# Kernel optimization log

Hardware: AMD Instinct MI355X
Metric: run time of the kernel (lower is better)

## Reference

```python
import jax, jax.numpy as jnp
import numpy as np

N = 131072          # events
N_OBS = 64          # observables
HID = [512, 512, 512]          # trunk hidden widths
SUB_HID = [512, 256]           # per-pair subnetwork hidden widths
P = 3                          # number of pairings


def _glorot(key, shape):
    fan_in, fan_out = shape[-2], shape[-1]
    lim = np.sqrt(6.0 / (fan_in + fan_out)).astype(np.float32)
    return jax.random.uniform(key, shape, jnp.float32, -lim, lim)


def setup_inputs() -> dict:
    key = jax.random.key(0)
    ks = jax.random.split(key, 16)
    x = jax.random.normal(ks[0], (N, N_OBS), jnp.float32)
    y = jax.random.randint(ks[1], (N,), 0, 3)
    pairs = jnp.array([[0, 1], [0, 2], [1, 2]], dtype=jnp.int32)
    # trunk params
    W0 = _glorot(ks[2], (N_OBS, HID[0])); b0 = jnp.zeros((HID[0],), jnp.float32)
    W1 = _glorot(ks[3], (HID[0], HID[1])); b1 = jnp.zeros((HID[1],), jnp.float32)
    W2 = _glorot(ks[4], (HID[1], HID[2])); b2 = jnp.zeros((HID[2],), jnp.float32)
    # stacked per-pair subnetwork params (all P subnets share shapes)
    SW0 = _glorot(ks[5], (P, HID[2], SUB_HID[0])); Sb0 = jnp.zeros((P, SUB_HID[0]), jnp.float32)
    SW1 = _glorot(ks[6], (P, SUB_HID[0], SUB_HID[1])); Sb1 = jnp.zeros((P, SUB_HID[1]), jnp.float32)
    SW2 = _glorot(ks[7], (P, SUB_HID[1], 1)); Sb2 = jnp.zeros((P, 1), jnp.float32)
    return {"x": x, "y": y, "pairs": pairs,
            "W0": W0, "b0": b0, "W1": W1, "b1": b1, "W2": W2, "b2": b2,
            "SW0": SW0, "Sb0": Sb0, "SW1": SW1, "Sb1": Sb1, "SW2": SW2, "Sb2": Sb2}


def reference(x, y, pairs, W0, b0, W1, b1, W2, b2, SW0, Sb0, SW1, Sb1, SW2, Sb2):
    relu = jax.nn.relu
    # Trunk. Note: in the torch module with dropout_prob>0, the first Linear sits at
    # layer index 1, so the activation is applied to the raw input as well (eval-mode
    # dropout == identity). We reproduce that exactly.
    h = relu(x) @ W0 + b0
    h = relu(h) @ W1 + b1
    repr_ = relu(h) @ W2 + b2                      # [N, HID[-1]]

    # Per-pair membership masks (jit-safe stand-in for the variable-size gather):
    # mask[p, n] = True iff y[n] is one of the two labels of pairing p.
    mask = (y[None, :] == pairs[:, 0:1]) | (y[None, :] == pairs[:, 1:2])  # [P, N] bool

    # Per-pair RatioModel subnetworks, batched over the pair dim.
    # Same activation-before-every-Linear pattern as the trunk (dropout indices).
    hs = jnp.einsum('nd,pdh->pnh', relu(repr_), SW0) + Sb0[:, None, :]
    hs = jnp.einsum('pnh,phk->pnk', relu(hs), SW1) + Sb1[:, None, :]
    logit = jnp.einsum('pnk,pko->pno', relu(hs), SW2) + Sb2[:, None, :]  # [P, N, 1]
    s_hat = jnp.clip(jax.nn.sigmoid(logit[..., 0]), 1e-9, None)          # [P, N]
    r_hat = (1.0 - s_hat) / s_hat                                        # [P, N]

    maskf = mask.astype(s_hat.dtype)
    return repr_, r_hat * maskf, s_hat * maskf, mask
```

## Files before the change

kernel.cpp:

```cpp
#include <hip/hip_runtime.h>
#include <stdint.h>

#define NE 131072

typedef __attribute__((ext_vector_type(8))) short bf16x8;
typedef __attribute__((ext_vector_type(4))) float f32x4;

static __device__ __forceinline__ unsigned short f2bf(float f) {
  unsigned u = __float_as_uint(f);
  u += 0x7FFF + ((u >> 16) & 1);
  return (unsigned short)(u >> 16);
}
static __device__ __forceinline__ float bf2f(unsigned short h) {
  return __uint_as_float((unsigned)h << 16);
}
static __device__ __forceinline__ void gload_lds16(const void* g, void* l) {
  __builtin_amdgcn_global_load_lds(
      (const __attribute__((address_space(1))) unsigned*)g,
      (__attribute__((address_space(3))) unsigned*)l, 16, 0, 0);
}

__global__ void weight_prep(const float* __restrict__ W0, const float* __restrict__ W1,
                            const float* __restrict__ W2, const float* __restrict__ SW0,
                            const float* __restrict__ SW1, const float* __restrict__ SW2,
                            unsigned short* W0t, unsigned short* W1t,
                            unsigned short* W2t, unsigned short* SW0t,
                            unsigned short* SW1t, unsigned short* SW2b) {
  __shared__ float tile[32][33];
  const int u = blockIdx.y;
  const float* src; unsigned short* dst; int K, Nc;
  if (u == 0)      { src = W0;  dst = W0t;  K = 64;  Nc = 512; }
  else if (u == 1) { src = W1;  dst = W1t;  K = 512; Nc = 512; }
  else if (u == 2) { src = W2;  dst = W2t;  K = 512; Nc = 512; }
  else if (u < 6)  { int p = u - 3; src = SW0 + (long)p * 512 * 512; dst = SW0t + (long)p * 512 * 512; K = 512; Nc = 512; }
  else if (u < 9)  { int p = u - 6; src = SW1 + (long)p * 512 * 256; dst = SW1t + (long)p * 256 * 512; K = 512; Nc = 256; }
  else             { int p = u - 9; src = SW2 + (long)p * 256;       dst = SW2b + (long)p * 256;       K = 256; Nc = 1; }
  const int tkn = K >> 5;
  const int tk = blockIdx.x % tkn, tn = blockIdx.x / tkn;
  if (tn >= ((Nc + 31) >> 5)) return;
  const int k0 = tk * 32, n0 = tn * 32;
  const int tx = threadIdx.x & 31, ty = threadIdx.x >> 5;
  if (n0 + tx < Nc)
#pragma unroll
    for (int j = 0; j < 4; ++j)
      tile[ty * 4 + j][tx] = src[(long)(k0 + ty * 4 + j) * Nc + n0 + tx];
  __syncthreads();
#pragma unroll
  for (int j = 0; j < 4; ++j) {
    int n = n0 + ty * 4 + j;
    if (n < Nc) dst[(long)n * K + k0 + tx] = f2bf(tile[tx][ty * 4 + j]);
  }
}

__global__ void relu_cvt_x(const float4* __restrict__ x,
                           ushort4* __restrict__ xb) {
  int i = blockIdx.x * blockDim.x + threadIdx.x;
  float4 v = x[i];
  ushort4 o;
  o.x = f2bf(fmaxf(v.x, 0.f));
  o.y = f2bf(fmaxf(v.y, 0.f));
  o.z = f2bf(fmaxf(v.z, 0.f));
  o.w = f2bf(fmaxf(v.w, 0.f));
  xb[i] = o;
}

__global__ __launch_bounds__(512, 4) void gemmP(
    const unsigned short* __restrict__ A, long aZ,
    const unsigned short* __restrict__ Bt, long bZ,
    const float* __restrict__ bias, long biasZ,
    float* __restrict__ outF,
    unsigned short* __restrict__ outA, long cZ,
    int K, int Nc,
    const unsigned short* __restrict__ w2, long w2Z,
    float* __restrict__ PB, long pbZ, int r0) {
  __shared__ unsigned short lds[3 * 12288];
  __shared__ float part[4][256];
  const int z = blockIdx.z;
  A += (long)z * aZ;
  Bt += (long)z * bZ;
  bias += (long)z * biasZ;
  if (outA) outA += (long)z * cZ;
  if (w2) { w2 += (long)z * w2Z; PB += (long)z * pbZ; }

  const int tid = threadIdx.x, wave = tid >> 6, lane = tid & 63;
  const int wm = wave >> 2, wn = wave & 3;
  const int lr = lane & 15, lh = lane >> 4;
  const long brow = (long)blockIdx.x * 256;
  const int bcol = blockIdx.y * 128;
  const int nk = K >> 5;
  const int axr = (lh ^ ((lr >> 1) & 3)) * 8;

  f32x4 acc[8][2];
#pragma unroll
  for (int m = 0; m < 8; ++m)
#pragma unroll
    for (int n = 0; n < 2; ++n) acc[m][n] = (f32x4){0.f, 0.f, 0.f, 0.f};

  auto STAGE = [&](int t) {
    if (t >= nk) return;
    unsigned short* dst = &lds[(t % 3) * 12288];
    const int k0 = t << 5;
#pragma unroll
    for (int i = 0; i < 2; ++i) {
      const int cb = i * 512 + wave * 64;
      const int c = cb + lane;
      const int r = c >> 2;
      const int kc = (c & 3) ^ ((r >> 1) & 3);
      gload_lds16(A + (brow + r) * (long)K + k0 + kc * 8, &dst[cb * 8]);
    }
    {
      const int cb = wave * 64;
      const int c = cb + lane;
      const int r = c >> 2;
      const int kc = (c & 3) ^ ((r >> 1) & 3);
      gload_lds16(Bt + (long)(bcol + r) * K + k0 + kc * 8,
                  &dst[(1024 + cb) * 8]);
    }
  };

  STAGE(0);
  STAGE(1);

  for (int t = 0; t < nk; ++t) {
    if (t < nk - 1)
      asm volatile("s_waitcnt vmcnt(3)" ::: "memory");
    else
      asm volatile("s_waitcnt vmcnt(0)" ::: "memory");
    __builtin_amdgcn_s_barrier();
    __builtin_amdgcn_sched_barrier(0);
    const unsigned short* buf = &lds[(t % 3) * 12288];
    bf16x8 a[8], b[2];
#pragma unroll
    for (int m = 0; m < 8; ++m)
      a[m] = *(const bf16x8*)&buf[(wm * 128 + m * 16 + lr) * 32 + axr];
#pragma unroll
    for (int n = 0; n < 2; ++n)
      b[n] = *(const bf16x8*)&buf[1024 * 8 + (wn * 32 + n * 16 + lr) * 32 + axr];
    STAGE(t + 2);
    __builtin_amdgcn_s_setprio(1);
#pragma unroll
    for (int m = 0; m < 8; ++m)
#pragma unroll
      for (int n = 0; n < 2; ++n)
        acc[m][n] =
            __builtin_amdgcn_mfma_f32_16x16x32_bf16(a[m], b[n], acc[m][n], 0, 0, 0);
    __builtin_amdgcn_s_setprio(0);
  }

  float bv[2];
#pragma unroll
  for (int n = 0; n < 2; ++n) bv[n] = bias[bcol + wn * 32 + n * 16 + lr];

  if (!w2) {
#pragma unroll
    for (int m = 0; m < 8; ++m) {
#pragma unroll
      for (int r = 0; r < 4; ++r) {
        long e = brow + wm * 128 + m * 16 + lh * 4 + r;
#pragma unroll
        for (int n = 0; n < 2; ++n) {
          int oc = bcol + wn * 32 + n * 16 + lr;
          float v = acc[m][n][r] + bv[n];
          if (outF) outF[e * Nc + oc] = v;
          if (outA) outA[e * Nc + oc] = f2bf(fmaxf(v, 0.f));
        }
      }
    }
  } else {
    float w2v[2];
#pragma unroll
    for (int n = 0; n < 2; ++n) w2v[n] = bf2f(w2[bcol + wn * 32 + n * 16 + lr]);
#pragma unroll
    for (int m = 0; m < 8; ++m) {
#pragma unroll
      for (int r = 0; r < 4; ++r) {
        float s = 0.f;
#pragma unroll
        for (int n = 0; n < 2; ++n)
          s += fmaxf(acc[m][n][r] + bv[n], 0.f) * w2v[n];
#pragma unroll
        for (int off = 1; off < 16; off <<= 1) s += __shfl_xor(s, off);
        if (lr == 0) part[wn][wm * 128 + m * 16 + lh * 4 + r] = s;
      }
    }
    __syncthreads();
    if (tid < 256)
      PB[(long)blockIdx.y * NE + r0 + brow + tid] =
          part[0][tid] + part[1][tid] + part[2][tid] + part[3][tid];
  }
}

__global__ void head_final(const float* __restrict__ PB,
                           const float* __restrict__ Sb2,
                           const int* __restrict__ y,
                           const int* __restrict__ pairs,
                           float* __restrict__ outR, float* __restrict__ outS,
                           float* __restrict__ outM) {
  const int n = blockIdx.x * 256 + threadIdx.x;
  const int p = blockIdx.y;
  float logit = PB[(long)p * 2 * NE + n] + PB[(long)(p * 2 + 1) * NE + n] +
                Sb2[p];
  float s = 1.f / (1.f + expf(-logit));
  s = fmaxf(s, 1e-9f);
  float r = (1.f - s) / s;
  int yv = y[n];
  float mf = (yv == pairs[p * 2] || yv == pairs[p * 2 + 1]) ? 1.f : 0.f;
  outR[(long)p * NE + n] = r * mf;
  outS[(long)p * NE + n] = s * mf;
  outM[(long)p * NE + n] = mf;
}

extern "C" void kernel_launch(void* const* d_in, const int* in_sizes, int n_in,
                              void* d_out, int out_size, void* d_ws, size_t ws_size,
                              hipStream_t stream) {
  const float* x   = (const float*)d_in[0];
  const int*   y   = (const int*)d_in[1];
  const int*   prs = (const int*)d_in[2];
  const float* W0  = (const float*)d_in[3];
  const float* b0  = (const float*)d_in[4];
  const float* W1  = (const float*)d_in[5];
  const float* b1  = (const float*)d_in[6];
  const float* W2  = (const float*)d_in[7];
  const float* b2  = (const float*)d_in[8];
  const float* SW0 = (const float*)d_in[9];
  const float* Sb0 = (const float*)d_in[10];
  const float* SW1 = (const float*)d_in[11];
  const float* Sb1 = (const float*)d_in[12];
  const float* SW2 = (const float*)d_in[13];
  const float* Sb2 = (const float*)d_in[14];

  uint8_t* ws = (uint8_t*)d_ws;
  size_t off = 0;
  auto take = [&](size_t bytes) -> void* {
    void* ptr = ws + off;
    off = (off + bytes + 255) & ~(size_t)255;
    return ptr;
  };
  unsigned short* W0t  = (unsigned short*)take((size_t)64 * 512 * 2);
  unsigned short* W1t  = (unsigned short*)take((size_t)512 * 512 * 2);
  unsigned short* W2t  = (unsigned short*)take((size_t)512 * 512 * 2);
  unsigned short* SW0t = (unsigned short*)take((size_t)3 * 512 * 512 * 2);
  unsigned short* SW1t = (unsigned short*)take((size_t)3 * 256 * 512 * 2);
  unsigned short* SW2b = (unsigned short*)take((size_t)3 * 256 * 2);
  unsigned short* Xb   = (unsigned short*)take((size_t)NE * 64 * 2);
  float*          PB   = (float*)take((size_t)6 * NE * 4);
  const size_t fixed = off;

  long chunk = 32768;
  while (chunk > 8192 && fixed + (size_t)6 * chunk * 1024 + 4096 > ws_size)
    chunk >>= 1;

  unsigned short* T0   = (unsigned short*)take((size_t)chunk * 512 * 2);
  unsigned short* T1   = (unsigned short*)take((size_t)chunk * 512 * 2);
  unsigned short* bufR = (unsigned short*)take((size_t)chunk * 512 * 2);
  unsigned short* H3   = (unsigned short*)take((size_t)3 * chunk * 512 * 2);

  float* out   = (float*)d_out;
  float* outRe = out;
  float* outR  = out + (size_t)NE * 512;
  float* outS  = outR + (size_t)3 * NE;
  float* outM  = outS + (size_t)3 * NE;

  weight_prep<<<dim3(256, 12), 256, 0, stream>>>(W0, W1, W2, SW0, SW1, SW2,
                                                 W0t, W1t, W2t, SW0t, SW1t, SW2b);
  relu_cvt_x<<<dim3(NE * 64 / 4 / 256), 256, 0, stream>>>((const float4*)x,
                                                          (ushort4*)Xb);

  for (long r0 = 0; r0 < NE; r0 += chunk) {
    gemmP<<<dim3(chunk / 256, 4, 1), 512, 0, stream>>>(
        Xb + r0 * 64, 0, W0t, 0, b0, 0, nullptr, T0, 0, 64, 512,
        nullptr, 0, nullptr, 0, 0);
    gemmP<<<dim3(chunk / 256, 4, 1), 512, 0, stream>>>(
        T0, 0, W1t, 0, b1, 0, nullptr, T1, 0, 512, 512,
        nullptr, 0, nullptr, 0, 0);
    gemmP<<<dim3(chunk / 256, 4, 1), 512, 0, stream>>>(
        T1, 0, W2t, 0, b2, 0, outRe + r0 * 512, bufR, 0, 512, 512,
        nullptr, 0, nullptr, 0, 0);
    gemmP<<<dim3(chunk / 256, 4, 3), 512, 0, stream>>>(
        bufR, 0, SW0t, (long)512 * 512, Sb0, 512, nullptr,
        H3, (long)chunk * 512, 512, 512,
        nullptr, 0, nullptr, 0, 0);
    gemmP<<<dim3(chunk / 256, 2, 3), 512, 0, stream>>>(
        H3, (long)chunk * 512, SW1t, (long)256 * 512, Sb1, 256, nullptr,
        nullptr, 0, 512, 256,
        SW2b, 256, PB, (long)2 * NE, (int)r0);
  }
  head_final<<<dim3(NE / 256, 3), 256, 0, stream>>>(PB, Sb2, y, prs,
                                                    outR, outS, outM);
}
```

Measured before the change: 705.6 us.

## Add 256x256-tile GEMM kernel with interleaved staging for K=512 layers

Introduces gemmQ, a GEMM using a 256x256 output tile per block (8 waves, each 128x64) with double-buffered LDS filled by direct global-to-LDS loads, XOR-swizzled rows, and load stages interleaved between MFMA phases with s_setprio. It replaces the 256x128-style gemmP launches for the trunk layers 1-2 and the first subnet layer, halving the grid's column dimension. The aim is more data reuse per loaded tile and better overlap of memory with MFMA work; the cost is larger register pressure (128 accumulator floats per thread), 128KB LDS per block limiting occupancy, and fewer blocks in flight.

```diff
diff --git a/kernel.cpp b/kernel.cpp
--- a/kernel.cpp
+++ b/kernel.cpp
@@ -190,6 +190,147 @@
   }
 }
 
+#define MFMA16(MQ, N0)                                                       \
+  _Pragma("unroll") for (int m = 0; m < 4; ++m)                              \
+  _Pragma("unroll") for (int n = 0; n < 2; ++n)                              \
+  _Pragma("unroll") for (int kk = 0; kk < 2; ++kk)                           \
+      acc[(MQ)*4 + m][(N0) + n] = __builtin_amdgcn_mfma_f32_16x16x32_bf16(   \
+          a[m][kk], b[(N0) + n][kk], acc[(MQ)*4 + m][(N0) + n], 0, 0, 0);
+
+__global__ __launch_bounds__(512) void gemmQ(
+    const unsigned short* __restrict__ A, long aZ,
+    const unsigned short* __restrict__ Bt, long bZ,
+    const float* __restrict__ bias, long biasZ,
+    float* __restrict__ outF,
+    unsigned short* __restrict__ outA, long cZ,
+    int K, int Nc) {
+  __shared__ unsigned short lds[65536];
+  const int z = blockIdx.z;
+  A += (long)z * aZ;
+  Bt += (long)z * bZ;
+  bias += (long)z * biasZ;
+  if (outA) outA += (long)z * cZ;
+
+  const int tid = threadIdx.x;
+  const int wave = tid >> 6, lane = tid & 63;
+  const int wm = wave >> 2, wn = wave & 3;
+  const int lr = lane & 15, lh = lane >> 4;
+  const long brow = (long)blockIdx.x * 256;
+  const int bcol = blockIdx.y * 256;
+  const int nk = K >> 6;
+
+  f32x4 acc[8][4];
+#pragma unroll
+  for (int m = 0; m < 8; ++m)
+#pragma unroll
+    for (int n = 0; n < 4; ++n) acc[m][n] = (f32x4){0.f, 0.f, 0.f, 0.f};
+
+  auto STAGE = [&](int S) {
+    if (S >= nk * 4) return;
+    const int tile = S >> 2, slot = S & 3, buf = tile & 1, half = slot & 1;
+    const int k0 = tile << 6;
+    const unsigned short* src;
+    long rb;
+    int lbase;
+    if (slot >= 2) {
+      src = A;  rb = brow + half * 128;  lbase = buf * 16384 + half * 8192;
+    } else {
+      src = Bt; rb = bcol + half * 128;  lbase = 32768 + buf * 16384 + half * 8192;
+    }
+#pragma unroll
+    for (int i = 0; i < 2; ++i) {
+      const int c = i * 512 + wave * 64 + lane;
+      const int row = c >> 3, sl = c & 7;
+      const int kc = sl ^ (row & 7);
+      gload_lds16(src + (rb + row) * (long)K + k0 + kc * 8,
+                  &lds[lbase + c * 8]);
+    }
+  };
+
+#pragma unroll
+  for (int S0 = 0; S0 < 7; ++S0) STAGE(S0);
+  asm volatile("s_waitcnt vmcnt(6)" ::: "memory");
+  __builtin_amdgcn_s_barrier();
+
+  const int rs0 = (0 * 4 + lh) ^ (lr & 7);
+  const int rs1 = (1 * 4 + lh) ^ (lr & 7);
+
+  bf16x8 a[4][2], b[4][2];
+  int S = 7;
+  for (int t = 0; t < nk; ++t) {
+    const int buf = t & 1;
+    const char* ab = (const char*)&lds[buf * 16384 + wm * 8192];
+    const char* bb =
+        (const char*)&lds[32768 + buf * 16384 + (wn >> 1) * 8192 +
+                          (wn & 1) * 64 * 64];
+#pragma unroll
+    for (int m = 0; m < 4; ++m) {
+      const int row = m * 16 + lr;
+      a[m][0] = *(const bf16x8*)(ab + row * 128 + rs0 * 16);
+      a[m][1] = *(const bf16x8*)(ab + row * 128 + rs1 * 16);
+    }
+#pragma unroll
+    for (int n = 0; n < 4; ++n) {
+      const int row = n * 16 + lr;
+      b[n][0] = *(const bf16x8*)(bb + row * 128 + rs0 * 16);
+      b[n][1] = *(const bf16x8*)(bb + row * 128 + rs1 * 16);
+    }
+    STAGE(S++);
+    __builtin_amdgcn_s_barrier();
+    __builtin_amdgcn_s_setprio(1);
+    MFMA16(0, 0)
+    __builtin_amdgcn_s_setprio(0);
+    __builtin_amdgcn_s_barrier();
+    STAGE(S++);
+    __builtin_amdgcn_s_barrier();
+    __builtin_amdgcn_s_setprio(1);
+    MFMA16(0, 2)
+    __builtin_amdgcn_s_setprio(0);
+    __builtin_amdgcn_s_barrier();
+#pragma unroll
+    for (int m = 0; m < 4; ++m) {
+      const int row = 64 + m * 16 + lr;
+      a[m][0] = *(const bf16x8*)(ab + row * 128 + rs0 * 16);
+      a[m][1] = *(const bf16x8*)(ab + row * 128 + rs1 * 16);
+    }
+    STAGE(S++);
+    __builtin_amdgcn_s_barrier();
+    __builtin_amdgcn_s_setprio(1);
+    MFMA16(1, 2)
+    __builtin_amdgcn_s_setprio(0);
+    __builtin_amdgcn_s_barrier();
+    STAGE(S++);
+    if (t < nk - 2)
+      asm volatile("s_waitcnt vmcnt(6)" ::: "memory");
+    else
+      asm volatile("s_waitcnt vmcnt(0)" ::: "memory");
+    __builtin_amdgcn_s_barrier();
+    __builtin_amdgcn_s_setprio(1);
+    MFMA16(1, 0)
+    __builtin_amdgcn_s_setprio(0);
+    __builtin_amdgcn_s_barrier();
+  }
+
+  float bv[4];
+#pragma unroll
+  for (int n = 0; n < 4; ++n) bv[n] = bias[bcol + wn * 64 + n * 16 + lr];
+#pragma unroll
+  for (int m = 0; m < 8; ++m) {
+    long rbase = brow + wm * 128 + m * 16 + lh * 4;
+#pragma unroll
+    for (int r = 0; r < 4; ++r) {
+      long rr = rbase + r;
+#pragma unroll
+      for (int n = 0; n < 4; ++n) {
+        int cc = bcol + wn * 64 + n * 16 + lr;
+        float v = acc[m][n][r] + bv[n];
+        if (outF) outF[rr * Nc + cc] = v;
+        if (outA) outA[rr * Nc + cc] = f2bf(fmaxf(v, 0.f));
+      }
+    }
+  }
+}
+
 __global__ void head_final(const float* __restrict__ PB,
                            const float* __restrict__ Sb2,
                            const int* __restrict__ y,
@@ -270,16 +411,13 @@
     gemmP<<<dim3(chunk / 256, 4, 1), 512, 0, stream>>>(
         Xb + r0 * 64, 0, W0t, 0, b0, 0, nullptr, T0, 0, 64, 512,
         nullptr, 0, nullptr, 0, 0);
-    gemmP<<<dim3(chunk / 256, 4, 1), 512, 0, stream>>>(
-        T0, 0, W1t, 0, b1, 0, nullptr, T1, 0, 512, 512,
-        nullptr, 0, nullptr, 0, 0);
-    gemmP<<<dim3(chunk / 256, 4, 1), 512, 0, stream>>>(
-        T1, 0, W2t, 0, b2, 0, outRe + r0 * 512, bufR, 0, 512, 512,
-        nullptr, 0, nullptr, 0, 0);
-    gemmP<<<dim3(chunk / 256, 4, 3), 512, 0, stream>>>(
+    gemmQ<<<dim3(chunk / 256, 2, 1), 512, 0, stream>>>(
+        T0, 0, W1t, 0, b1, 0, nullptr, T1, 0, 512, 512);
+    gemmQ<<<dim3(chunk / 256, 2, 1), 512, 0, stream>>>(
+        T1, 0, W2t, 0, b2, 0, outRe + r0 * 512, bufR, 0, 512, 512);
+    gemmQ<<<dim3(chunk / 256, 2, 3), 512, 0, stream>>>(
         bufR, 0, SW0t, (long)512 * 512, Sb0, 512, nullptr,
-        H3, (long)chunk * 512, 512, 512,
-        nullptr, 0, nullptr, 0, 0);
+        H3, (long)chunk * 512, 512, 512);
     gemmP<<<dim3(chunk / 256, 2, 3), 512, 0, stream>>>(
         H3, (long)chunk * 512, SW1t, (long)256 * 512, Sb1, 256, nullptr,
         nullptr, 0, 512, 256,
```

After: 729.4 us. +3.4%, slower.

## Compact per-pair rows and skip subnetwork GEMMs for masked-out events

Applied to the files above, without the earlier changes.

Adds a kernel that builds per-chunk, per-pair compacted index lists of events whose label belongs to the pairing, plus a reverse position map. The subnetwork GEMMs gather input rows through this index and exit early for row blocks past the padded active count, so events whose outputs are zeroed by the mask are not computed. The head kernel reads logits through the position map and writes zeros for inactive events. This adds a serial scan kernel and indirect row loads in exchange for skipping roughly a third of the subnetwork work.

```diff
diff --git a/kernel.cpp b/kernel.cpp
--- a/kernel.cpp
+++ b/kernel.cpp
@@ -64,6 +64,49 @@
   xb[i] = o;
 }
 
+__global__ void build_idx(const int* __restrict__ y, const int* __restrict__ pairs,
+                          int chunkRows, int* __restrict__ idxL,
+                          int* __restrict__ posA, int* __restrict__ cnts) {
+  const int c = blockIdx.x, p = blockIdx.y;
+  const int la = pairs[p * 2], lb = pairs[p * 2 + 1];
+  const long r0 = (long)c * chunkRows;
+  const long cb = r0;
+  __shared__ int wbase[4];
+  __shared__ int running;
+  if (threadIdx.x == 0) running = 0;
+  __syncthreads();
+  const int lane = threadIdx.x & 63, wv = threadIdx.x >> 6;
+  for (int it = 0; it < chunkRows / 256; ++it) {
+    const int r = it * 256 + threadIdx.x;
+    const int yv = y[r0 + r];
+    const bool act = (yv == la) || (yv == lb);
+    const unsigned long long m = __ballot(act);
+    const int rank = __popcll(m & ((1ull << lane) - 1));
+    if (lane == 0) wbase[wv] = __popcll(m);
+    __syncthreads();
+    int wb = 0;
+#pragma unroll
+    for (int w = 0; w < 4; ++w) wb += (w < wv) ? wbase[w] : 0;
+    const int tot = wbase[0] + wbase[1] + wbase[2] + wbase[3];
+    if (act) {
+      const int posi = running + wb + rank;
+      idxL[(long)p * NE + cb + posi] = r;
+      posA[(long)p * NE + r0 + r] = (int)(cb + posi);
+    } else {
+      posA[(long)p * NE + r0 + r] = -1;
+    }
+    __syncthreads();
+    if (threadIdx.x == 0) running += tot;
+    __syncthreads();
+  }
+  const int cnt = running;
+  if (threadIdx.x == 0) cnts[c * 3 + p] = cnt;
+  const int padded = (cnt + 255) & ~255;
+  const int last = (cnt > 0) ? idxL[(long)p * NE + cb + cnt - 1] : 0;
+  for (int i = cnt + threadIdx.x; i < padded; i += 256)
+    idxL[(long)p * NE + cb + i] = last;
+}
+
 __global__ __launch_bounds__(512, 4) void gemmP(
     const unsigned short* __restrict__ A, long aZ,
     const unsigned short* __restrict__ Bt, long bZ,
@@ -72,23 +115,38 @@
     unsigned short* __restrict__ outA, long cZ,
     int K, int Nc,
     const unsigned short* __restrict__ w2, long w2Z,
-    float* __restrict__ PB, long pbZ, int r0) {
+    float* __restrict__ PB, long pbZ, int r0,
+    const int* __restrict__ aIdx, long aIdxZ,
+    const int* __restrict__ cnts) {
   __shared__ unsigned short lds[3 * 12288];
   __shared__ float part[4][256];
   const int z = blockIdx.z;
+  const long brow = (long)blockIdx.x * 256;
+  if (cnts) {
+    const int cp = cnts[z];
+    if ((int)brow >= ((cp + 255) & ~255)) return;
+  }
   A += (long)z * aZ;
   Bt += (long)z * bZ;
   bias += (long)z * biasZ;
   if (outA) outA += (long)z * cZ;
   if (w2) { w2 += (long)z * w2Z; PB += (long)z * pbZ; }
+  if (aIdx) aIdx += (long)z * aIdxZ;
 
   const int tid = threadIdx.x, wave = tid >> 6, lane = tid & 63;
   const int wm = wave >> 2, wn = wave & 3;
   const int lr = lane & 15, lh = lane >> 4;
-  const long brow = (long)blockIdx.x * 256;
   const int bcol = blockIdx.y * 128;
   const int nk = K >> 5;
   const int axr = (lh ^ ((lr >> 1) & 3)) * 8;
+
+  int arow[2];
+#pragma unroll
+  for (int i = 0; i < 2; ++i) {
+    const int c = i * 512 + wave * 64 + lane;
+    const int r = c >> 2;
+    arow[i] = aIdx ? aIdx[brow + r] : (int)(brow + r);
+  }
 
   f32x4 acc[8][2];
 #pragma unroll
@@ -106,7 +164,7 @@
       const int c = cb + lane;
       const int r = c >> 2;
       const int kc = (c & 3) ^ ((r >> 1) & 3);
-      gload_lds16(A + (brow + r) * (long)K + k0 + kc * 8, &dst[cb * 8]);
+      gload_lds16(A + (long)arow[i] * K + k0 + kc * 8, &dst[cb * 8]);
     }
     {
       const int cb = wave * 64;
@@ -191,22 +249,24 @@
 }
 
 __global__ void head_final(const float* __restrict__ PB,
+                           const int* __restrict__ posA,
                            const float* __restrict__ Sb2,
-                           const int* __restrict__ y,
-                           const int* __restrict__ pairs,
                            float* __restrict__ outR, float* __restrict__ outS,
                            float* __restrict__ outM) {
-  const int n = blockIdx.x * 256 + threadIdx.x;
+  const long n = (long)blockIdx.x * 256 + threadIdx.x;
   const int p = blockIdx.y;
-  float logit = PB[(long)p * 2 * NE + n] + PB[(long)(p * 2 + 1) * NE + n] +
-                Sb2[p];
-  float s = 1.f / (1.f + expf(-logit));
-  s = fmaxf(s, 1e-9f);
-  float r = (1.f - s) / s;
-  int yv = y[n];
-  float mf = (yv == pairs[p * 2] || yv == pairs[p * 2 + 1]) ? 1.f : 0.f;
-  outR[(long)p * NE + n] = r * mf;
-  outS[(long)p * NE + n] = s * mf;
+  const int pos = posA[(long)p * NE + n];
+  float rr = 0.f, s = 0.f, mf = 0.f;
+  if (pos >= 0) {
+    float logit = PB[(long)p * 2 * NE + pos] + PB[((long)p * 2 + 1) * NE + pos] +
+                  Sb2[p];
+    s = 1.f / (1.f + expf(-logit));
+    s = fmaxf(s, 1e-9f);
+    rr = (1.f - s) / s;
+    mf = 1.f;
+  }
+  outR[(long)p * NE + n] = rr;
+  outS[(long)p * NE + n] = s;
   outM[(long)p * NE + n] = mf;
 }
 
@@ -244,11 +304,15 @@
   unsigned short* SW2b = (unsigned short*)take((size_t)3 * 256 * 2);
   unsigned short* Xb   = (unsigned short*)take((size_t)NE * 64 * 2);
   float*          PB   = (float*)take((size_t)6 * NE * 4);
+  int*            idxL = (int*)take((size_t)3 * NE * 4);
+  int*            posA = (int*)take((size_t)3 * NE * 4);
+  int*            cnts = (int*)take((size_t)64 * 4);
   const size_t fixed = off;
 
   long chunk = 32768;
   while (chunk > 8192 && fixed + (size_t)6 * chunk * 1024 + 4096 > ws_size)
     chunk >>= 1;
+  const int nchunks = (int)(NE / chunk);
 
   unsigned short* T0   = (unsigned short*)take((size_t)chunk * 512 * 2);
   unsigned short* T1   = (unsigned short*)take((size_t)chunk * 512 * 2);
@@ -265,26 +329,29 @@
                                                  W0t, W1t, W2t, SW0t, SW1t, SW2b);
   relu_cvt_x<<<dim3(NE * 64 / 4 / 256), 256, 0, stream>>>((const float4*)x,
                                                           (ushort4*)Xb);
-
-  for (long r0 = 0; r0 < NE; r0 += chunk) {
+  build_idx<<<dim3(nchunks, 3), 256, 0, stream>>>(y, prs, (int)chunk,
+                                                  idxL, posA, cnts);
+
+  for (int c = 0; c < nchunks; ++c) {
+    const long r0 = (long)c * chunk;
     gemmP<<<dim3(chunk / 256, 4, 1), 512, 0, stream>>>(
         Xb + r0 * 64, 0, W0t, 0, b0, 0, nullptr, T0, 0, 64, 512,
-        nullptr, 0, nullptr, 0, 0);
+        nullptr, 0, nullptr, 0, 0, nullptr, 0, nullptr);
     gemmP<<<dim3(chunk / 256, 4, 1), 512, 0, stream>>>(
         T0, 0, W1t, 0, b1, 0, nullptr, T1, 0, 512, 512,
-        nullptr, 0, nullptr, 0, 0);
+        nullptr, 0, nullptr, 0, 0, nullptr, 0, nullptr);
     gemmP<<<dim3(chunk / 256, 4, 1), 512, 0, stream>>>(
         T1, 0, W2t, 0, b2, 0, outRe + r0 * 512, bufR, 0, 512, 512,
-        nullptr, 0, nullptr, 0, 0);
+        nullptr, 0, nullptr, 0, 0, nullptr, 0, nullptr);
     gemmP<<<dim3(chunk / 256, 4, 3), 512, 0, stream>>>(
         bufR, 0, SW0t, (long)512 * 512, Sb0, 512, nullptr,
         H3, (long)chunk * 512, 512, 512,
-        nullptr, 0, nullptr, 0, 0);
+        nullptr, 0, nullptr, 0, 0, idxL + r0, NE, cnts + c * 3);
     gemmP<<<dim3(chunk / 256, 2, 3), 512, 0, stream>>>(
         H3, (long)chunk * 512, SW1t, (long)256 * 512, Sb1, 256, nullptr,
         nullptr, 0, 512, 256,
-        SW2b, 256, PB, (long)2 * NE, (int)r0);
-  }
-  head_final<<<dim3(NE / 256, 3), 256, 0, stream>>>(PB, Sb2, y, prs,
+        SW2b, 256, PB, (long)2 * NE, (int)r0, nullptr, 0, cnts + c * 3);
+  }
+  head_final<<<dim3(NE / 256, 3), 256, 0, stream>>>(PB, posA, Sb2,
                                                     outR, outS, outM);
 }
```

Result: no change. 718.0 us (+1.8%).
